# Kernel tuning notes

Hardware: AMD Instinct MI355X
Metric: run time of the kernel (lower is better)

Reference implementation:

```python
import jax, jax.numpy as jnp
import numpy as np

IN, H, OUT, R, E, B = 4096, 4096, 4096, 512, 4, 64
TOT = R * IN + H * R + R * H + OUT * R  # 8388608


def setup_inputs() -> dict:
    key = jax.random.key(0)
    ks = jax.random.split(key, 7)
    s = 0.02
    x = jax.random.normal(ks[0], (B, IN), jnp.float32)
    scores = jax.random.uniform(ks[1], (E,), jnp.float32)
    delta = jax.random.normal(ks[2], (E, 1, TOT), jnp.float32) * s
    # single shared expert's base weights (all experts alias the same module)
    W1 = jax.random.normal(ks[3], (R, IN), jnp.float32) * s   # hidden_layer_u.weight
    W2 = jax.random.normal(ks[4], (H, R), jnp.float32) * s    # hidden_layer_v.weight
    W3 = jax.random.normal(ks[5], (R, H), jnp.float32) * s    # output_layer_u.weight
    W4 = jax.random.normal(ks[6], (OUT, R), jnp.float32) * s  # output_layer_v.weight
    return {"x": x, "scores": scores, "delta": delta, "W1": W1, "W2": W2, "W3": W3, "W4": W4}


def reference(x, scores, delta, W1, W2, W3, W4):
    # slice flat per-expert deltas into the four weight deltas
    d = delta[:, 0, :]                                   # [E, TOT]
    j = 0
    d1 = d[:, j:j + R * IN].reshape(E, R, IN); j += R * IN
    d2 = d[:, j:j + H * R].reshape(E, H, R);   j += H * R
    d3 = d[:, j:j + R * H].reshape(E, R, H);   j += R * H
    d4 = d[:, j:j + OUT * R].reshape(E, OUT, R)
    Wa = W1[None] + d1   # [E, R, IN]
    Wb = W2[None] + d2   # [E, H, R]
    Wc = W3[None] + d3   # [E, R, H]
    Wd = W4[None] + d4   # [E, OUT, R]
    h = jnp.einsum('bi,eri->ebr', x, Wa)                 # F.linear with W1+d1
    h = jnp.einsum('ebr,ehr->ebh', h, Wb)                # F.linear with W2+d2
    h = jax.nn.relu(h)
    h = jnp.einsum('ebh,erh->ebr', h, Wc)                # F.linear with W3+d3
    h = jnp.einsum('ebr,eor->ebo', h, Wd)                # F.linear with W4+d4
    return jnp.einsum('ebo,e->bo', h, scores)            # score-weighted sum over experts
```

## Files before the change

### kernel.cpp

```cpp
#include <hip/hip_runtime.h>
#include <hip/hip_bf16.h>

#define E_N 4
#define B_N 64
#define IN_N 4096
#define H_N 4096
#define R_N 512
#define OUT_N 4096
#define TOT_N 8388608

typedef float f32x4 __attribute__((ext_vector_type(4)));
typedef short bf16x8 __attribute__((ext_vector_type(8)));
typedef unsigned short u16x8 __attribute__((ext_vector_type(8)));

__device__ __forceinline__ unsigned short f2bf_bits(float f) {
    return __builtin_bit_cast(unsigned short, __float2bfloat16(f));
}
__device__ __forceinline__ float bfbits2f(unsigned short u) {
    return __builtin_bit_cast(float, ((unsigned)u) << 16);
}

__device__ __forceinline__ void stage16(const void* g, void* l) {
    __builtin_amdgcn_global_load_lds(
        (const __attribute__((address_space(1))) void*)g,
        (__attribute__((address_space(3))) void*)l, 16, 0, 0);
}

template<int K_TOT, int N_TOT, int KS, bool A_SHARED, bool RELU, bool OUT_BF16>
__global__ __launch_bounds__(256, 2)
void gemm_layer(const __hip_bfloat16* __restrict__ A, const float* __restrict__ W,
                const float* __restrict__ D, float* __restrict__ OutF,
                __hip_bfloat16* __restrict__ OutB)
{
    constexpr int KCH = K_TOT / KS;
    constexpr int NT = N_TOT / 32;
    constexpr int NTILES = KCH / 64;
    __shared__ float Wt[32][64];
    __shared__ float Dt[32][64];
    __shared__ __hip_bfloat16 At[64][64];

    const int bid = blockIdx.x;
    const int ks = bid % KS;
    const int nt = (bid / KS) % NT;
    const int e  = bid / (KS * NT);
    const int tid = threadIdx.x;
    const int l  = tid & 63;
    const int w  = tid >> 6;
    const int wn = w & 1;
    const int wm = w >> 1;
    const int lr = l & 15;
    const int lk = (l >> 4) << 3;

    const float* Wb = W + (size_t)(nt * 32) * K_TOT + ks * KCH;
    const float* Db = D + (size_t)e * TOT_N + (size_t)(nt * 32) * K_TOT + ks * KCH;
    const __hip_bfloat16* Ab = A + (A_SHARED ? (size_t)0 : (size_t)e * B_N * K_TOT)
                                 + ks * KCH;

    const char* gsrc[6];
    char* ldst[6];
    int kstep[6];
    #pragma unroll
    for (int i = 0; i < 6; ++i) {
        const int q = w * 6 + i;
        if (q < 8) {
            const int off = q * 1024 + l * 16;
            const int row = off >> 8;
            const int kb  = off & 255;
            const int skb = kb ^ ((row & 7) << 4);
            gsrc[i] = (const char*)(Wb + (size_t)row * K_TOT) + skb;
            ldst[i] = (char*)&Wt[0][0] + q * 1024;
            kstep[i] = 4;
        } else if (q < 16) {
            const int c = q - 8;
            const int off = c * 1024 + l * 16;
            const int row = off >> 8;
            const int kb  = off & 255;
            const int skb = kb ^ ((row & 7) << 4);
            gsrc[i] = (const char*)(Db + (size_t)row * K_TOT) + skb;
            ldst[i] = (char*)&Dt[0][0] + c * 1024;
            kstep[i] = 4;
        } else {
            const int c = q - 16;
            const int off = c * 1024 + l * 16;
            const int row = off >> 7;
            const int kb  = off & 127;
            const int skb = kb ^ ((row & 7) << 4);
            gsrc[i] = (const char*)(Ab + (size_t)row * K_TOT) + skb;
            ldst[i] = (char*)&At[0][0] + c * 1024;
            kstep[i] = 2;
        }
    }

    f32x4 acc[2] = {};
    const int wrow = wn * 16 + lr;
    const int wswz = (wrow & 7) << 4;
    const int arow0 = wm * 32 + lr;
    const int aswz = (arow0 & 7) << 4;

    for (int t = 0; t < NTILES; ++t) {
        const int kk = t * 64;
        #pragma unroll
        for (int i = 0; i < 6; ++i)
            stage16(gsrc[i] + kk * kstep[i], ldst[i]);
        __syncthreads();

        #pragma unroll
        for (int inner = 0; inner < 2; ++inner) {
            const int b0 = (inner * 32 + lk) * 4;
            const char* wrp = (const char*)&Wt[0][0] + wrow * 256;
            const char* drp = (const char*)&Dt[0][0] + wrow * 256;
            f32x4 w0 = *(const f32x4*)(wrp + ((b0)      ^ wswz));
            f32x4 w1 = *(const f32x4*)(wrp + ((b0 + 16) ^ wswz));
            f32x4 d0 = *(const f32x4*)(drp + ((b0)      ^ wswz));
            f32x4 d1 = *(const f32x4*)(drp + ((b0 + 16) ^ wswz));
            f32x4 s0 = w0 + d0;
            f32x4 s1 = w1 + d1;
            bf16x8 bhi, blo;
            #pragma unroll
            for (int j = 0; j < 4; ++j) {
                unsigned short h0 = f2bf_bits(s0[j]);
                bhi[j] = (short)h0;
                blo[j] = (short)f2bf_bits(s0[j] - bfbits2f(h0));
                unsigned short h1 = f2bf_bits(s1[j]);
                bhi[j + 4] = (short)h1;
                blo[j + 4] = (short)f2bf_bits(s1[j] - bfbits2f(h1));
            }
            const int ab = (inner * 32 + lk) * 2;
            #pragma unroll
            for (int mf = 0; mf < 2; ++mf) {
                const int ar = arow0 + mf * 16;
                const char* arp = (const char*)&At[0][0] + ar * 128;
                bf16x8 af = *(const bf16x8*)(arp + (ab ^ aswz));
                acc[mf] = __builtin_amdgcn_mfma_f32_16x16x32_bf16(af, bhi, acc[mf], 0, 0, 0);
                acc[mf] = __builtin_amdgcn_mfma_f32_16x16x32_bf16(af, blo, acc[mf], 0, 0, 0);
            }
        }
        __syncthreads();
    }

    const int rb = (l >> 4) * 4;
    const int nrow = nt * 32 + wrow;
    #pragma unroll
    for (int j = 0; j < 2; ++j) {
        #pragma unroll
        for (int i = 0; i < 4; ++i) {
            const int row = wm * 32 + j * 16 + rb + i;
            float v = acc[j][i];
            if (RELU) v = fmaxf(v, 0.0f);
            if (OUT_BF16) {
                OutB[(size_t)e * B_N * N_TOT + (size_t)row * N_TOT + nrow] =
                    __float2bfloat16(v);
            } else {
                OutF[(size_t)(e * KS + ks) * B_N * N_TOT + (size_t)row * N_TOT + nrow] = v;
            }
        }
    }
}

template<int KS, int TOTAL, int BN>
__global__ __launch_bounds__(256)
void reduce_ks_bf16(const float* __restrict__ P, __hip_bfloat16* __restrict__ H)
{
    const int t = blockIdx.x * blockDim.x + threadIdx.x;
    const int idx = t * 8;
    const int e = idx / BN;
    const int r = idx - e * BN;
    const float* base = P + (size_t)e * KS * BN + r;
    f32x4 s0 = {}, s1 = {};
    #pragma unroll
    for (int k = 0; k < KS; ++k) {
        s0 += *(const f32x4*)(base + (size_t)k * BN);
        s1 += *(const f32x4*)(base + (size_t)k * BN + 4);
    }
    u16x8 o;
    #pragma unroll
    for (int j = 0; j < 4; ++j) {
        o[j]     = f2bf_bits(s0[j]);
        o[j + 4] = f2bf_bits(s1[j]);
    }
    *(u16x8*)(H + idx) = o;
}

__global__ __launch_bounds__(256)
void convert_bf16(const float* __restrict__ X, __hip_bfloat16* __restrict__ Xb)
{
    const int t = blockIdx.x * blockDim.x + threadIdx.x;
    const int idx = t * 8;
    f32x4 a0 = *(const f32x4*)(X + idx);
    f32x4 a1 = *(const f32x4*)(X + idx + 4);
    u16x8 o;
    #pragma unroll
    for (int j = 0; j < 4; ++j) {
        o[j]     = f2bf_bits(a0[j]);
        o[j + 4] = f2bf_bits(a1[j]);
    }
    *(u16x8*)(Xb + idx) = o;
}

__global__ __launch_bounds__(256)
void reduce_experts(const float* __restrict__ P, const float* __restrict__ scores,
                    float* __restrict__ out)
{
    const int t = blockIdx.x * blockDim.x + threadIdx.x;
    const int idx = t * 4;
    f32x4 acc = {};
    #pragma unroll
    for (int e = 0; e < E_N; ++e) {
        f32x4 v = *(const f32x4*)(P + (size_t)e * (B_N * OUT_N) + idx);
        acc += scores[e] * v;
    }
    *(f32x4*)(out + idx) = acc;
}

extern "C" void kernel_launch(void* const* d_in, const int* in_sizes, int n_in,
                              void* d_out, int out_size, void* d_ws, size_t ws_size,
                              hipStream_t stream)
{
    const float* x      = (const float*)d_in[0];
    const float* scores = (const float*)d_in[1];
    const float* delta  = (const float*)d_in[2];
    const float* W1     = (const float*)d_in[3];
    const float* W2     = (const float*)d_in[4];
    const float* W3     = (const float*)d_in[5];
    const float* W4     = (const float*)d_in[6];
    float* out = (float*)d_out;

    char* ws = (char*)d_ws;
    __hip_bfloat16* xb  = (__hip_bfloat16*)(ws);
    __hip_bfloat16* h1b = (__hip_bfloat16*)(ws + 524288);
    __hip_bfloat16* h2b = (__hip_bfloat16*)(ws + 786432);
    __hip_bfloat16* h3b = (__hip_bfloat16*)(ws + 2883584);
    float* P1 = (float*)(ws + 3145728);
    float* P3 = (float*)(ws + 7340032);
    float* P4 = (float*)(ws + 11534336);

    const float* d1 = delta;
    const float* d2 = d1 + (size_t)R_N * IN_N;
    const float* d3 = d2 + (size_t)H_N * R_N;
    const float* d4 = d3 + (size_t)R_N * H_N;

    convert_bf16<<<dim3(B_N * IN_N / 8 / 256), dim3(256), 0, stream>>>(x, xb);

    gemm_layer<IN_N, R_N, 8, true, false, false>
        <<<dim3(E_N * (R_N / 32) * 8), dim3(256), 0, stream>>>(xb, W1, d1, P1, nullptr);
    reduce_ks_bf16<8, E_N * B_N * R_N, B_N * R_N>
        <<<dim3(E_N * B_N * R_N / 8 / 256), dim3(256), 0, stream>>>(P1, h1b);

    gemm_layer<R_N, H_N, 1, false, true, true>
        <<<dim3(E_N * (H_N / 32)), dim3(256), 0, stream>>>(h1b, W2, d2, nullptr, h2b);

    gemm_layer<H_N, R_N, 8, false, false, false>
        <<<dim3(E_N * (R_N / 32) * 8), dim3(256), 0, stream>>>(h2b, W3, d3, P3, nullptr);
    reduce_ks_bf16<8, E_N * B_N * R_N, B_N * R_N>
        <<<dim3(E_N * B_N * R_N / 8 / 256), dim3(256), 0, stream>>>(P3, h3b);

    gemm_layer<R_N, OUT_N, 1, false, false, false>
        <<<dim3(E_N * (OUT_N / 32)), dim3(256), 0, stream>>>(h3b, W4, d4, P4, nullptr);

    reduce_experts<<<dim3(B_N * OUT_N / 4 / 256), dim3(256), 0, stream>>>(P4, scores, out);
}
```

Measured before the change: 56.67 us.

## Double-buffer LDS tiles to overlap global-to-LDS staging with MFMA compute

Replaces the single set of W, D and A shared tiles with two ping-pong LDS buffers and prefetches the next K tile while computing on the current one. It drops the barrier between staging and compute, relying on the end-of-iteration barrier to make prefetched data visible. This aims to hide global load latency behind the conversion and MFMA work. LDS use per block doubles, which could limit occupancy.

```diff
diff --git a/kernel.cpp b/kernel.cpp
--- a/kernel.cpp
+++ b/kernel.cpp
@@ -35,9 +35,8 @@
     constexpr int KCH = K_TOT / KS;
     constexpr int NT = N_TOT / 32;
     constexpr int NTILES = KCH / 64;
-    __shared__ float Wt[32][64];
-    __shared__ float Dt[32][64];
-    __shared__ __hip_bfloat16 At[64][64];
+    constexpr int BUFSZ = 24576;
+    __shared__ __align__(16) char smem[2 * BUFSZ];
 
     const int bid = blockIdx.x;
     const int ks = bid % KS;
@@ -57,7 +56,7 @@
                                  + ks * KCH;
 
     const char* gsrc[6];
-    char* ldst[6];
+    int loff[6];
     int kstep[6];
     #pragma unroll
     for (int i = 0; i < 6; ++i) {
@@ -66,27 +65,24 @@
             const int off = q * 1024 + l * 16;
             const int row = off >> 8;
             const int kb  = off & 255;
-            const int skb = kb ^ ((row & 7) << 4);
-            gsrc[i] = (const char*)(Wb + (size_t)row * K_TOT) + skb;
-            ldst[i] = (char*)&Wt[0][0] + q * 1024;
+            gsrc[i] = (const char*)(Wb + (size_t)row * K_TOT) + (kb ^ ((row & 7) << 4));
+            loff[i] = q * 1024;
             kstep[i] = 4;
         } else if (q < 16) {
             const int c = q - 8;
             const int off = c * 1024 + l * 16;
             const int row = off >> 8;
             const int kb  = off & 255;
-            const int skb = kb ^ ((row & 7) << 4);
-            gsrc[i] = (const char*)(Db + (size_t)row * K_TOT) + skb;
-            ldst[i] = (char*)&Dt[0][0] + c * 1024;
+            gsrc[i] = (const char*)(Db + (size_t)row * K_TOT) + (kb ^ ((row & 7) << 4));
+            loff[i] = 8192 + c * 1024;
             kstep[i] = 4;
         } else {
             const int c = q - 16;
             const int off = c * 1024 + l * 16;
             const int row = off >> 7;
             const int kb  = off & 127;
-            const int skb = kb ^ ((row & 7) << 4);
-            gsrc[i] = (const char*)(Ab + (size_t)row * K_TOT) + skb;
-            ldst[i] = (char*)&At[0][0] + c * 1024;
+            gsrc[i] = (const char*)(Ab + (size_t)row * K_TOT) + (kb ^ ((row & 7) << 4));
+            loff[i] = 16384 + c * 1024;
             kstep[i] = 2;
         }
     }
@@ -97,18 +93,26 @@
     const int arow0 = wm * 32 + lr;
     const int aswz = (arow0 & 7) << 4;
 
+    #pragma unroll
+    for (int i = 0; i < 6; ++i)
+        stage16(gsrc[i], smem + loff[i]);
+    __syncthreads();
+
     for (int t = 0; t < NTILES; ++t) {
-        const int kk = t * 64;
-        #pragma unroll
-        for (int i = 0; i < 6; ++i)
-            stage16(gsrc[i] + kk * kstep[i], ldst[i]);
-        __syncthreads();
-
+        if (t + 1 < NTILES) {
+            const int kk = (t + 1) * 64;
+            char* b = smem + ((t + 1) & 1) * BUFSZ;
+            #pragma unroll
+            for (int i = 0; i < 6; ++i)
+                stage16(gsrc[i] + kk * kstep[i], b + loff[i]);
+        }
+
+        const char* buf = smem + (t & 1) * BUFSZ;
         #pragma unroll
         for (int inner = 0; inner < 2; ++inner) {
             const int b0 = (inner * 32 + lk) * 4;
-            const char* wrp = (const char*)&Wt[0][0] + wrow * 256;
-            const char* drp = (const char*)&Dt[0][0] + wrow * 256;
+            const char* wrp = buf + wrow * 256;
+            const char* drp = buf + 8192 + wrow * 256;
             f32x4 w0 = *(const f32x4*)(wrp + ((b0)      ^ wswz));
             f32x4 w1 = *(const f32x4*)(wrp + ((b0 + 16) ^ wswz));
             f32x4 d0 = *(const f32x4*)(drp + ((b0)      ^ wswz));
@@ -129,7 +133,7 @@
             #pragma unroll
             for (int mf = 0; mf < 2; ++mf) {
                 const int ar = arow0 + mf * 16;
-                const char* arp = (const char*)&At[0][0] + ar * 128;
+                const char* arp = buf + 16384 + ar * 128;
                 bf16x8 af = *(const bf16x8*)(arp + (ab ^ aswz));
                 acc[mf] = __builtin_amdgcn_mfma_f32_16x16x32_bf16(af, bhi, acc[mf], 0, 0, 0);
                 acc[mf] = __builtin_amdgcn_mfma_f32_16x16x32_bf16(af, blo, acc[mf], 0, 0, 0);
```

Result: faster. 51.56 us (-9.0%).
